# Performance work log

Measured on AMD Instinct MI355X. Metric: run time of the kernel, lower is better.

The kernel has to match this reference:

```python
import jax, jax.numpy as jnp
import numpy as np

B, N, D, D_MODEL = 4, 2048, 512, 512


def setup_inputs() -> dict:
    key = jax.random.key(0)
    kx, kq, kk, kv, ks = jax.random.split(key, 5)
    scale = 1.0 / np.sqrt(D)
    x = jax.random.normal(kx, (B, N, D), dtype=jnp.float32)
    Wq = (jax.random.normal(kq, (D, D_MODEL), dtype=jnp.float32) * scale)
    Wk = (jax.random.normal(kk, (D, D_MODEL), dtype=jnp.float32) * scale)
    Wv = (jax.random.normal(kv, (D, D_MODEL), dtype=jnp.float32) * scale)
    Ws = (jax.random.normal(ks, (D, 1), dtype=jnp.float32) * scale)
    return {"x": x, "Wq": Wq, "Wk": Wk, "Wv": Wv, "Ws": Ws}


def reference(x, Wq, Wk, Wv, Ws):
    # Projections (Linear, no bias)
    Q = x @ Wq                      # (B, N, d_model)
    K = x @ Wk                      # (B, N, d_model)
    V = x @ Wv                      # (B, N, d_model)
    sigma = x @ Ws                  # (B, N, 1)

    n = x.shape[1]
    dm = Wq.shape[1]

    # Prior association: Gaussian kernel over |i-j| distance, row-normalized
    idx = jnp.arange(n)
    dist = jnp.abs(idx[:, None] - idx[None, :]).astype(x.dtype)      # (N, N)
    inv_norm = 1.0 / (jnp.sqrt(2.0 * jnp.pi).astype(x.dtype) * jnp.abs(sigma))
    gaussian = inv_norm * jnp.exp(-0.5 * jnp.square(dist[None] / sigma))  # (B,N,N)
    P = gaussian / jnp.sum(gaussian, axis=-1, keepdims=True)

    # Series association: scaled dot-product softmax attention
    scores = jnp.einsum('bnd,bmd->bnm', Q, K) / jnp.sqrt(jnp.asarray(dm, x.dtype))
    S = jax.nn.softmax(scores, axis=-1)                               # (B,N,N)

    # Reconstruction
    Z = S @ V                                                          # (B,N,d_model)
    return (Z, P)
```

## Files before the change

kernel.cpp:

```cpp
#include <hip/hip_runtime.h>

typedef float f32x4 __attribute__((ext_vector_type(4)));
typedef short s16x8 __attribute__((ext_vector_type(8)));
typedef unsigned short us4 __attribute__((ext_vector_type(4)));

#define MFMA16(a, b, c) __builtin_amdgcn_mfma_f32_16x16x32_bf16(a, b, c, 0, 0, 0)

#define GLOAD_LDS16(gp, lp) __builtin_amdgcn_global_load_lds( \
    (__attribute__((address_space(1))) void*)(gp),            \
    (__attribute__((address_space(3))) void*)(lp), 16, 0, 0)

__device__ __forceinline__ unsigned short f2bf(float f) {
    union { float f; unsigned u; } v; v.f = f;
    unsigned r = v.u + 0x7fffu + ((v.u >> 16) & 1u);
    return (unsigned short)(r >> 16);
}

#define RP 136
#define SH128 (128 * RP)

__device__ __forceinline__ void gemm_core128_db(
    const unsigned short* __restrict__ Ab, size_t Astride,
    const unsigned short* __restrict__ Bb, size_t Bstride,
    int K, unsigned short* sh, int t, f32x4 acc[4][4])
{
    const int wave = t >> 6, lane = t & 63;
    const int c = lane & 15, quad = lane >> 4;
    const int wm = (wave >> 1) * 64, wn = (wave & 1) * 64;
    const int srow = t >> 2;
    const int scol = (t & 3) * 8;

    const unsigned short* ga = Ab + (size_t)srow * Astride + scol;
    const unsigned short* gb = Bb + (size_t)srow * Bstride + scol;

    GLOAD_LDS16(ga,                 sh + t * 8);
    GLOAD_LDS16(ga + 64 * Astride,  sh + 2048 + t * 8);
    GLOAD_LDS16(gb,                 sh + 4096 + t * 8);
    GLOAD_LDS16(gb + 64 * Bstride,  sh + 4096 + 2048 + t * 8);
    __syncthreads();

    int cur = 0;
    for (int k0 = 0; k0 < K; k0 += 32) {
        const unsigned short* buf = sh + cur * 8192;
        if (k0 + 32 < K) {
            unsigned short* nb = sh + (cur ^ 1) * 8192;
            GLOAD_LDS16(ga + k0 + 32,                 nb + t * 8);
            GLOAD_LDS16(ga + k0 + 32 + 64 * Astride,  nb + 2048 + t * 8);
            GLOAD_LDS16(gb + k0 + 32,                 nb + 4096 + t * 8);
            GLOAD_LDS16(gb + k0 + 32 + 64 * Bstride,  nb + 4096 + 2048 + t * 8);
        }
        s16x8 af[4], bf[4];
        #pragma unroll
        for (int i = 0; i < 4; i++)
            af[i] = *(const s16x8*)(buf + (wm + i * 16 + c) * 32 + quad * 8);
        #pragma unroll
        for (int i = 0; i < 4; i++)
            bf[i] = *(const s16x8*)(buf + 4096 + (wn + i * 16 + c) * 32 + quad * 8);
        #pragma unroll
        for (int mt = 0; mt < 4; mt++)
            #pragma unroll
            for (int nt = 0; nt < 4; nt++)
                acc[mt][nt] = MFMA16(af[mt], bf[nt], acc[mt][nt]);
        __syncthreads();
        cur ^= 1;
    }
}

__global__ __launch_bounds__(256) void k_convert(
    const float* __restrict__ x, const float* __restrict__ wq,
    const float* __restrict__ wk, const float* __restrict__ wv,
    unsigned short* __restrict__ xbf, unsigned short* __restrict__ wt)
{
    __shared__ __align__(16) unsigned short lt[64][72];

    int bid = blockIdx.x, t = threadIdx.x;
    if (bid < 4096) {
        int gid = bid * 256 + t;
        float4 v = ((const float4*)x)[gid];
        us4 o = { f2bf(v.x), f2bf(v.y), f2bf(v.z), f2bf(v.w) };
        ((us4*)xbf)[gid] = o;
    } else {
        int idx = bid - 4096;
        int w = idx >> 6;
        int tile = idx & 63;
        int tk = tile >> 3, tn = tile & 7;
        const float* src = ((w == 0) ? wq : (w == 1) ? wk : wv)
                         + (size_t)(tk * 64) * 512 + tn * 64;

        int row = t >> 2;
        int c0 = (t & 3) * 16;
        const float4* s = (const float4*)(src + (size_t)row * 512 + c0);
        #pragma unroll
        for (int q = 0; q < 4; q++) {
            float4 v = s[q];
            lt[c0 + q * 4 + 0][row] = f2bf(v.x);
            lt[c0 + q * 4 + 1][row] = f2bf(v.y);
            lt[c0 + q * 4 + 2][row] = f2bf(v.z);
            lt[c0 + q * 4 + 3][row] = f2bf(v.w);
        }
        __syncthreads();

        int n = t >> 2;
        int k0 = (t & 3) * 16;
        s16x8 a = *(const s16x8*)&lt[n][k0];
        s16x8 b = *(const s16x8*)&lt[n][k0 + 8];
        unsigned short* dst = wt + (((size_t)(w * 512 + tn * 64 + n)) << 9)
                                 + tk * 64 + k0;
        *(s16x8*)dst = a;
        *(s16x8*)(dst + 8) = b;
    }
}

__global__ __launch_bounds__(256) void k_proj(
    const unsigned short* __restrict__ xbf, const unsigned short* __restrict__ wt,
    unsigned short* __restrict__ qbf, unsigned short* __restrict__ kbf,
    unsigned short* __restrict__ vtbf)
{
    __shared__ __align__(16) unsigned short sh[SH128];

    int t = threadIdx.x;
    int m0 = blockIdx.x * 128, n0 = blockIdx.y * 128;
    f32x4 acc[4][4] = {};

    gemm_core128_db(xbf + (size_t)m0 * 512, 512, wt + (size_t)n0 * 512, 512,
                    512, sh, t, acc);

    int wave = t >> 6, lane = t & 63, c = lane & 15, quad = lane >> 4;
    int wm = (wave >> 1) * 64, wn = (wave & 1) * 64;
    int sel = blockIdx.y >> 2;

    if (sel < 2) {
        unsigned short* dst = sel ? kbf : qbf;
        int ncol0 = n0 - sel * 512;
        #pragma unroll
        for (int mt = 0; mt < 4; mt++)
            #pragma unroll
            for (int nt = 0; nt < 4; nt++)
                #pragma unroll
                for (int r = 0; r < 4; r++)
                    sh[(wm + mt * 16 + quad * 4 + r) * RP + wn + nt * 16 + c]
                        = f2bf(acc[mt][nt][r]);
        __syncthreads();
        int rr = t >> 1, hh = (t & 1) * 64;
        const s16x8* sp = (const s16x8*)(sh + rr * RP + hh);
        s16x8* dp = (s16x8*)(dst + (size_t)(m0 + rr) * 512 + ncol0 + hh);
        s16x8 v[8];
        #pragma unroll
        for (int i = 0; i < 8; i++) v[i] = sp[i];
        #pragma unroll
        for (int i = 0; i < 8; i++) dp[i] = v[i];
    } else {
        #pragma unroll
        for (int mt = 0; mt < 4; mt++)
            #pragma unroll
            for (int nt = 0; nt < 4; nt++)
                #pragma unroll
                for (int r = 0; r < 4; r++)
                    sh[(wn + nt * 16 + c) * RP + wm + mt * 16 + quad * 4 + r]
                        = f2bf(acc[mt][nt][r]);
        __syncthreads();
        int bb = m0 >> 11, nn0 = m0 & 2047;
        int dbase = n0 - 1024;
        int dl = t >> 1, nh = (t & 1) * 64;
        const s16x8* sp = (const s16x8*)(sh + dl * RP + nh);
        s16x8* dp = (s16x8*)(vtbf + ((size_t)(bb * 512 + dbase + dl)) * 2048
                                  + nn0 + nh);
        s16x8 v[8];
        #pragma unroll
        for (int i = 0; i < 8; i++) v[i] = sp[i];
        #pragma unroll
        for (int i = 0; i < 8; i++) dp[i] = v[i];
    }
}

__device__ __forceinline__ void score_body(
    const unsigned short* __restrict__ qbf, const unsigned short* __restrict__ kbf,
    unsigned short* __restrict__ pbf,
    int b, int m0, int n0, int t, unsigned short* sh)
{
    f32x4 acc[4][4] = {};
    gemm_core128_db(qbf + (size_t)(b * 2048 + m0) * 512, 512,
                    kbf + (size_t)(b * 2048 + n0) * 512, 512,
                    512, sh, t, acc);

    int wave = t >> 6, lane = t & 63, c = lane & 15, quad = lane >> 4;
    int wm = (wave >> 1) * 64, wn = (wave & 1) * 64;
    const float scale = 0.044194173824159216f;

    #pragma unroll
    for (int mt = 0; mt < 4; mt++) {
        #pragma unroll
        for (int r = 0; r < 4; r++) {
            int row = wm + mt * 16 + quad * 4 + r;
            #pragma unroll
            for (int nt = 0; nt < 4; nt++) {
                float p = __expf(acc[mt][nt][r] * scale);
                sh[row * RP + wn + nt * 16 + c] = f2bf(p);
            }
        }
    }
    __syncthreads();
    int rr = t >> 1, hh = (t & 1) * 64;
    const s16x8* sp = (const s16x8*)(sh + rr * RP + hh);
    s16x8* dp = (s16x8*)(pbf + (size_t)(b * 2048 + m0 + rr) * 2048 + n0 + hh);
    s16x8 v[8];
    #pragma unroll
    for (int i = 0; i < 8; i++) v[i] = sp[i];
    #pragma unroll
    for (int i = 0; i < 8; i++) dp[i] = v[i];
}

__device__ __forceinline__ void prior_wave(
    const float* __restrict__ x, const float* __restrict__ wsv,
    float* __restrict__ pout, int row, int lane)
{
    const float4* xr = (const float4*)(x + (size_t)row * 512);
    const float4* wr = (const float4*)wsv;
    float4 a0 = xr[lane * 2],     b0 = wr[lane * 2];
    float4 a1 = xr[lane * 2 + 1], b1 = wr[lane * 2 + 1];
    float part = a0.x * b0.x + a0.y * b0.y + a0.z * b0.z + a0.w * b0.w
               + a1.x * b1.x + a1.y * b1.y + a1.z * b1.z + a1.w * b1.w;
    #pragma unroll
    for (int o = 32; o; o >>= 1) part += __shfl_xor(part, o, 64);
    float sigma = part;
    float inv2 = 0.5f / (sigma * sigma);

    int i = row & 2047;
    float g[32];
    float sum = 0.f;
    #pragma unroll
    for (int u = 0; u < 8; u++) {
        #pragma unroll
        for (int v = 0; v < 4; v++) {
            float d = (float)(u * 256 + lane * 4 + v - i);
            float e = __expf(-(d * d) * inv2);
            g[u * 4 + v] = e;
            sum += e;
        }
    }
    #pragma unroll
    for (int o = 32; o; o >>= 1) sum += __shfl_xor(sum, o, 64);
    float inv = 1.0f / sum;

    float4* pr = (float4*)(pout + (size_t)row * 2048);
    #pragma unroll
    for (int u = 0; u < 8; u++) {
        float4 o4 = { g[u * 4] * inv, g[u * 4 + 1] * inv,
                      g[u * 4 + 2] * inv, g[u * 4 + 3] * inv };
        pr[u * 64 + lane] = o4;
    }
}

__global__ __launch_bounds__(256) void k_score_prior(
    const unsigned short* __restrict__ qbf, const unsigned short* __restrict__ kbf,
    unsigned short* __restrict__ pbf,
    const float* __restrict__ x, const float* __restrict__ wsv,
    float* __restrict__ pout)
{
    __shared__ __align__(16) unsigned short sh[SH128];

    int bid = blockIdx.x, t = threadIdx.x;
    if (bid < 1024) {
        int b = bid >> 8, r = bid & 255;
        score_body(qbf, kbf, pbf, b, (r & 15) * 128, (r >> 4) * 128, t, sh);
    } else {
        int row = (bid - 1024) * 4 + (t >> 6);
        prior_wave(x, wsv, pout, row, t & 63);
    }
}

__global__ __launch_bounds__(256) void k_score(
    const unsigned short* __restrict__ qbf, const unsigned short* __restrict__ kbf,
    unsigned short* __restrict__ pbf)
{
    __shared__ __align__(16) unsigned short sh[SH128];
    score_body(qbf, kbf, pbf, blockIdx.z,
               blockIdx.x * 128, blockIdx.y * 128, threadIdx.x, sh);
}

__global__ __launch_bounds__(256) void k_out(
    const unsigned short* __restrict__ pbf, const unsigned short* __restrict__ vtbf,
    float* __restrict__ zout)
{
    __shared__ __align__(16) unsigned short sh[12288];

    int t = threadIdx.x;
    int b = blockIdx.z;
    int m0 = blockIdx.x * 128, n0 = blockIdx.y * 64;

    const int wave = t >> 6, lane = t & 63;
    const int c = lane & 15, quad = lane >> 4;
    const int wm = (wave >> 1) * 64, wn = (wave & 1) * 32;
    const int srow = t >> 2;
    const int scol = (t & 3) * 8;

    const unsigned short* ga = pbf + (size_t)(b * 2048 + m0 + srow) * 2048 + scol;
    const unsigned short* gb = vtbf + (size_t)(b * 512 + n0 + srow) * 2048 + scol;

    s16x8 ones;
    #pragma unroll
    for (int i = 0; i < 8; i++) ones[i] = (short)0x3F80;

    f32x4 acc[4][2] = {};
    f32x4 accl[4] = {};

    GLOAD_LDS16(ga,             sh + t * 8);
    GLOAD_LDS16(ga + 64 * 2048, sh + 2048 + t * 8);
    GLOAD_LDS16(gb,             sh + 4096 + t * 8);
    __syncthreads();

    int cur = 0;
    for (int k0 = 0; k0 < 2048; k0 += 32) {
        const unsigned short* buf = sh + cur * 6144;
        if (k0 + 32 < 2048) {
            unsigned short* nb = sh + (cur ^ 1) * 6144;
            GLOAD_LDS16(ga + k0 + 32,             nb + t * 8);
            GLOAD_LDS16(ga + k0 + 32 + 64 * 2048, nb + 2048 + t * 8);
            GLOAD_LDS16(gb + k0 + 32,             nb + 4096 + t * 8);
        }
        s16x8 af[4], bf[2];
        #pragma unroll
        for (int i = 0; i < 4; i++)
            af[i] = *(const s16x8*)(buf + (wm + i * 16 + c) * 32 + quad * 8);
        #pragma unroll
        for (int i = 0; i < 2; i++)
            bf[i] = *(const s16x8*)(buf + 4096 + (wn + i * 16 + c) * 32 + quad * 8);
        #pragma unroll
        for (int mt = 0; mt < 4; mt++) {
            #pragma unroll
            for (int nt = 0; nt < 2; nt++)
                acc[mt][nt] = MFMA16(af[mt], bf[nt], acc[mt][nt]);
            accl[mt] = MFMA16(af[mt], ones, accl[mt]);
        }
        __syncthreads();
        cur ^= 1;
    }

    #pragma unroll
    for (int mt = 0; mt < 4; mt++) {
        #pragma unroll
        for (int r = 0; r < 4; r++) {
            int row = wm + mt * 16 + quad * 4 + r;
            float inv = 1.0f / accl[mt][r];
            #pragma unroll
            for (int nt = 0; nt < 2; nt++) {
                zout[(size_t)(b * 2048 + m0 + row) * 512 + n0 + wn + nt * 16 + c]
                    = acc[mt][nt][r] * inv;
            }
        }
    }
}

__global__ __launch_bounds__(256) void k_prior(
    const float* __restrict__ x, const float* __restrict__ wsv,
    float* __restrict__ pout)
{
    int row = blockIdx.x * 4 + (threadIdx.x >> 6);
    prior_wave(x, wsv, pout, row, threadIdx.x & 63);
}

extern "C" void kernel_launch(void* const* d_in, const int* in_sizes, int n_in,
                              void* d_out, int out_size, void* d_ws, size_t ws_size,
                              hipStream_t stream)
{
    const float* x  = (const float*)d_in[0];
    const float* wq = (const float*)d_in[1];
    const float* wk = (const float*)d_in[2];
    const float* wv = (const float*)d_in[3];
    const float* ws = (const float*)d_in[4];

    float* zout = (float*)d_out;
    float* pout = zout + (size_t)4 * 2048 * 512;

    const size_t need = ((size_t)4194304 + 786432 + 3 * 4194304 + 16777216) * 2;

    if (ws_size >= need) {
        unsigned short* base = (unsigned short*)d_ws;
        unsigned short* xbf  = base;
        unsigned short* wt   = xbf  + (size_t)4194304;
        unsigned short* qbf  = wt   + (size_t)786432;
        unsigned short* kbf  = qbf  + (size_t)4194304;
        unsigned short* vtbf = kbf  + (size_t)4194304;
        unsigned short* pbf  = vtbf + (size_t)4194304;

        k_convert<<<dim3(4288), dim3(256), 0, stream>>>(x, wq, wk, wv, xbf, wt);
        k_proj       <<<dim3(64, 12),   dim3(256), 0, stream>>>(xbf, wt, qbf, kbf, vtbf);
        k_score_prior<<<dim3(3072),     dim3(256), 0, stream>>>(qbf, kbf, pbf, x, ws, pout);
        k_out        <<<dim3(16, 8, 4), dim3(256), 0, stream>>>(pbf, vtbf, zout);
    } else {
        unsigned short* base = (unsigned short*)pout;
        unsigned short* pbf  = base;
        unsigned short* qbf  = base + (size_t)16777216;
        unsigned short* kbf  = qbf  + (size_t)4194304;
        unsigned short* vtbf = kbf  + (size_t)4194304;
        unsigned short* xbf  = base;
        unsigned short* wt   = base + (size_t)4194304;

        k_convert<<<dim3(4288), dim3(256), 0, stream>>>(x, wq, wk, wv, xbf, wt);
        k_proj  <<<dim3(64, 12),    dim3(256), 0, stream>>>(xbf, wt, qbf, kbf, vtbf);
        k_score <<<dim3(16, 16, 4), dim3(256), 0, stream>>>(qbf, kbf, pbf);
        k_out   <<<dim3(16, 8, 4),  dim3(256), 0, stream>>>(pbf, vtbf, zout);
        k_prior <<<dim3(2048),      dim3(256), 0, stream>>>(x, ws, pout);
    }
}
```

Measured before the change: 199.1 us.

## Keep two LDS tile loads in flight with explicit vmcnt waits in GEMM loops

Reworks the double-buffered GEMM main loops (projection/score core and the PV kernel) so both buffers are prefetched up front. Each iteration then waits only on the older batch of global_load_lds operations via s_waitcnt vmcnt(N) instead of a full __syncthreads drain. The next refill is issued after the post-MFMA barrier into the buffer just consumed, so global loads overlap a whole iteration of compute. In exchange it depends on hand-written waitcnt counts and sched_barriers matching the compiler's instruction ordering, and it adds an extra barrier per iteration.

```diff
diff --git a/kernel.cpp b/kernel.cpp
--- a/kernel.cpp
+++ b/kernel.cpp
@@ -19,7 +19,7 @@
 #define RP 136
 #define SH128 (128 * RP)
 
-__device__ __forceinline__ void gemm_core128_db(
+__device__ __forceinline__ void gemm_core128_cnt(
     const unsigned short* __restrict__ Ab, size_t Astride,
     const unsigned short* __restrict__ Bb, size_t Bstride,
     int K, unsigned short* sh, int t, f32x4 acc[4][4])
@@ -36,19 +36,22 @@
     GLOAD_LDS16(ga,                 sh + t * 8);
     GLOAD_LDS16(ga + 64 * Astride,  sh + 2048 + t * 8);
     GLOAD_LDS16(gb,                 sh + 4096 + t * 8);
-    GLOAD_LDS16(gb + 64 * Bstride,  sh + 4096 + 2048 + t * 8);
-    __syncthreads();
+    GLOAD_LDS16(gb + 64 * Bstride,  sh + 6144 + t * 8);
+    if (32 < K) {
+        GLOAD_LDS16(ga + 32,                 sh + 8192 + t * 8);
+        GLOAD_LDS16(ga + 32 + 64 * Astride,  sh + 8192 + 2048 + t * 8);
+        GLOAD_LDS16(gb + 32,                 sh + 8192 + 4096 + t * 8);
+        GLOAD_LDS16(gb + 32 + 64 * Bstride,  sh + 8192 + 6144 + t * 8);
+    }
 
     int cur = 0;
     for (int k0 = 0; k0 < K; k0 += 32) {
+        if (k0 + 32 < K) asm volatile("s_waitcnt vmcnt(4)" ::: "memory");
+        else             asm volatile("s_waitcnt vmcnt(0)" ::: "memory");
+        __builtin_amdgcn_s_barrier();
+        __builtin_amdgcn_sched_barrier(0);
+
         const unsigned short* buf = sh + cur * 8192;
-        if (k0 + 32 < K) {
-            unsigned short* nb = sh + (cur ^ 1) * 8192;
-            GLOAD_LDS16(ga + k0 + 32,                 nb + t * 8);
-            GLOAD_LDS16(ga + k0 + 32 + 64 * Astride,  nb + 2048 + t * 8);
-            GLOAD_LDS16(gb + k0 + 32,                 nb + 4096 + t * 8);
-            GLOAD_LDS16(gb + k0 + 32 + 64 * Bstride,  nb + 4096 + 2048 + t * 8);
-        }
         s16x8 af[4], bf[4];
         #pragma unroll
         for (int i = 0; i < 4; i++)
@@ -56,12 +59,26 @@
         #pragma unroll
         for (int i = 0; i < 4; i++)
             bf[i] = *(const s16x8*)(buf + 4096 + (wn + i * 16 + c) * 32 + quad * 8);
+
+        asm volatile("s_waitcnt lgkmcnt(0)" ::: "memory");
+        __builtin_amdgcn_sched_barrier(0);
+
         #pragma unroll
         for (int mt = 0; mt < 4; mt++)
             #pragma unroll
             for (int nt = 0; nt < 4; nt++)
                 acc[mt][nt] = MFMA16(af[mt], bf[nt], acc[mt][nt]);
-        __syncthreads();
+
+        __builtin_amdgcn_s_barrier();
+        __builtin_amdgcn_sched_barrier(0);
+
+        if (k0 + 64 < K) {
+            unsigned short* nb = sh + cur * 8192;
+            GLOAD_LDS16(ga + k0 + 64,                 nb + t * 8);
+            GLOAD_LDS16(ga + k0 + 64 + 64 * Astride,  nb + 2048 + t * 8);
+            GLOAD_LDS16(gb + k0 + 64,                 nb + 4096 + t * 8);
+            GLOAD_LDS16(gb + k0 + 64 + 64 * Bstride,  nb + 6144 + t * 8);
+        }
         cur ^= 1;
     }
 }
@@ -122,8 +139,8 @@
     int m0 = blockIdx.x * 128, n0 = blockIdx.y * 128;
     f32x4 acc[4][4] = {};
 
-    gemm_core128_db(xbf + (size_t)m0 * 512, 512, wt + (size_t)n0 * 512, 512,
-                    512, sh, t, acc);
+    gemm_core128_cnt(xbf + (size_t)m0 * 512, 512, wt + (size_t)n0 * 512, 512,
+                     512, sh, t, acc);
 
     int wave = t >> 6, lane = t & 63, c = lane & 15, quad = lane >> 4;
     int wm = (wave >> 1) * 64, wn = (wave & 1) * 64;
@@ -179,9 +196,9 @@
     int b, int m0, int n0, int t, unsigned short* sh)
 {
     f32x4 acc[4][4] = {};
-    gemm_core128_db(qbf + (size_t)(b * 2048 + m0) * 512, 512,
-                    kbf + (size_t)(b * 2048 + n0) * 512, 512,
-                    512, sh, t, acc);
+    gemm_core128_cnt(qbf + (size_t)(b * 2048 + m0) * 512, 512,
+                     kbf + (size_t)(b * 2048 + n0) * 512, 512,
+                     512, sh, t, acc);
 
     int wave = t >> 6, lane = t & 63, c = lane & 15, quad = lane >> 4;
     int wm = (wave >> 1) * 64, wn = (wave & 1) * 64;
@@ -304,20 +321,21 @@
     f32x4 acc[4][2] = {};
     f32x4 accl[4] = {};
 
-    GLOAD_LDS16(ga,             sh + t * 8);
-    GLOAD_LDS16(ga + 64 * 2048, sh + 2048 + t * 8);
-    GLOAD_LDS16(gb,             sh + 4096 + t * 8);
-    __syncthreads();
+    GLOAD_LDS16(ga,                  sh + t * 8);
+    GLOAD_LDS16(ga + 64 * 2048,      sh + 2048 + t * 8);
+    GLOAD_LDS16(gb,                  sh + 4096 + t * 8);
+    GLOAD_LDS16(ga + 32,             sh + 6144 + t * 8);
+    GLOAD_LDS16(ga + 32 + 64 * 2048, sh + 6144 + 2048 + t * 8);
+    GLOAD_LDS16(gb + 32,             sh + 6144 + 4096 + t * 8);
 
     int cur = 0;
     for (int k0 = 0; k0 < 2048; k0 += 32) {
+        if (k0 + 32 < 2048) asm volatile("s_waitcnt vmcnt(3)" ::: "memory");
+        else                asm volatile("s_waitcnt vmcnt(0)" ::: "memory");
+        __builtin_amdgcn_s_barrier();
+        __builtin_amdgcn_sched_barrier(0);
+
         const unsigned short* buf = sh + cur * 6144;
-        if (k0 + 32 < 2048) {
-            unsigned short* nb = sh + (cur ^ 1) * 6144;
-            GLOAD_LDS16(ga + k0 + 32,             nb + t * 8);
-            GLOAD_LDS16(ga + k0 + 32 + 64 * 2048, nb + 2048 + t * 8);
-            GLOAD_LDS16(gb + k0 + 32,             nb + 4096 + t * 8);
-        }
         s16x8 af[4], bf[2];
         #pragma unroll
         for (int i = 0; i < 4; i++)
@@ -325,6 +343,10 @@
         #pragma unroll
         for (int i = 0; i < 2; i++)
             bf[i] = *(const s16x8*)(buf + 4096 + (wn + i * 16 + c) * 32 + quad * 8);
+
+        asm volatile("s_waitcnt lgkmcnt(0)" ::: "memory");
+        __builtin_amdgcn_sched_barrier(0);
+
         #pragma unroll
         for (int mt = 0; mt < 4; mt++) {
             #pragma unroll
@@ -332,7 +354,16 @@
                 acc[mt][nt] = MFMA16(af[mt], bf[nt], acc[mt][nt]);
             accl[mt] = MFMA16(af[mt], ones, accl[mt]);
         }
-        __syncthreads();
+
+        __builtin_amdgcn_s_barrier();
+        __builtin_amdgcn_sched_barrier(0);
+
+        if (k0 + 64 < 2048) {
+            unsigned short* nb = sh + cur * 6144;
+            GLOAD_LDS16(ga + k0 + 64,             nb + t * 8);
+            GLOAD_LDS16(ga + k0 + 64 + 64 * 2048, nb + 2048 + t * 8);
+            GLOAD_LDS16(gb + k0 + 64,             nb + 4096 + t * 8);
+        }
         cur ^= 1;
     }
 
```

Result: no change. 198.2 us (-0.5%).
